# Kernel tuning notes

Measured on AMD Instinct MI355X. Metric: run time of the kernel, lower is better.

The kernel has to match this reference:

```python
import jax, jax.numpy as jnp
import numpy as np

B, T, S, E, H, V, OOV = 16, 32, 400, 128, 512, 32000, 50


def setup_inputs() -> dict:
    key = jax.random.key(0)
    ks = jax.random.split(key, 24)
    sc = 0.05
    inp = {
        'input_embeddings': jax.random.normal(ks[0], (B, T, E), jnp.float32),
        'h0': jax.random.normal(ks[1], (B, H), jnp.float32) * sc,
        'c0': jax.random.normal(ks[2], (B, H), jnp.float32) * sc,
        'encoder_outputs': jax.random.normal(ks[3], (B, S, H), jnp.float32),
        'encoder_masks': jnp.ones((B, S), jnp.float32),
        'extra_zeros': jnp.zeros((B, OOV), jnp.float32),
        'extended_source_idx': jax.random.randint(ks[4], (B, S), 0, V + OOV),
        # LSTM cell params (torch gate order i,f,g,o)
        'W_ih': jax.random.normal(ks[5], (4 * H, E), jnp.float32) * sc,
        'W_hh': jax.random.normal(ks[6], (4 * H, H), jnp.float32) * sc,
        'b_ih': jax.random.normal(ks[7], (4 * H,), jnp.float32) * sc,
        'b_hh': jax.random.normal(ks[8], (4 * H,), jnp.float32) * sc,
        # vocab projection
        'W_vocab': jax.random.normal(ks[9], (V, H), jnp.float32) * sc,
        'b_vocab': jax.random.normal(ks[10], (V,), jnp.float32) * sc,
        # attention: coverage_linear (H,1), energy_linear (H, 2H), v (H)
        'W_cov': jax.random.normal(ks[11], (H, 1), jnp.float32) * sc,
        'W_energy': jax.random.normal(ks[12], (H, 2 * H), jnp.float32) * sc,
        'b_energy': jax.random.normal(ks[13], (H,), jnp.float32) * sc,
        'v_attn': jax.random.uniform(ks[14], (H,), jnp.float32),
        # x_context: (E, E+H)
        'W_xctx': jax.random.normal(ks[15], (E, E + H), jnp.float32) * sc,
        'b_xctx': jax.random.normal(ks[16], (E,), jnp.float32) * sc,
        # attention_dense: (H, 2H)
        'W_ad': jax.random.normal(ks[17], (H, 2 * H), jnp.float32) * sc,
        'b_ad': jax.random.normal(ks[18], (H,), jnp.float32) * sc,
        # p_gen: (1, H + H + E)
        'W_pgen': jax.random.normal(ks[19], (1, 2 * H + E), jnp.float32) * sc,
        'b_pgen': jax.random.normal(ks[20], (1,), jnp.float32) * sc,
    }
    return inp


def _forward(input_embeddings, h0, c0, encoder_outputs, encoder_masks, extra_zeros,
             W_ih, W_hh, b_ih, b_hh, W_vocab, b_vocab, W_cov, W_energy, b_energy,
             v_attn, W_xctx, b_xctx, W_ad, b_ad, W_pgen, b_pgen, extended_source_idx):
    Bc, Sc_, Hc = encoder_outputs.shape
    oov = extra_zeros.shape[1]
    # split energy linear into decoder-part and encoder-part (cat order: [dec, enc])
    W_d, W_e = W_energy[:, :Hc], W_energy[:, Hc:]
    # encoder projection computed ONCE (same math as per-step recompute)
    enc_proj = jnp.einsum('bsh,kh->bsk', encoder_outputs, W_e) + b_energy  # [B,S,H]
    w_cov = W_cov[:, 0]  # [H]
    rows = jnp.arange(Bc)[:, None]

    def step(carry, emb_t):
        h, c, ctx, cov = carry  # [B,H],[B,H],[B,H],[B,S]
        x = jnp.concatenate([emb_t, ctx], -1) @ W_xctx.T + b_xctx  # [B,E]
        gates = x @ W_ih.T + b_ih + h @ W_hh.T + b_hh
        i_g, f_g, g_g, o_g = jnp.split(gates, 4, axis=-1)
        c = jax.nn.sigmoid(f_g) * c + jax.nn.sigmoid(i_g) * jnp.tanh(g_g)
        h = jax.nn.sigmoid(o_g) * jnp.tanh(c)
        # additive attention with coverage
        dec_proj = h @ W_d.T  # [B,H]
        cov_feat = cov[:, :, None] * w_cov[None, None, :]  # [B,S,H]
        energy = jnp.tanh(dec_proj[:, None, :] + enc_proj + cov_feat)
        score = jnp.einsum('bsh,h->bs', energy, v_attn)
        probs = jax.nn.softmax(score, axis=-1) * encoder_masks
        probs = probs / (probs.sum(-1, keepdims=True) + 1e-12)
        ctx = jnp.einsum('bs,bsh->bh', probs, encoder_outputs)
        cov = cov + probs
        # vocab distribution
        hh = jnp.concatenate([h, ctx], -1) @ W_ad.T + b_ad
        vocab_dist = jax.nn.softmax(hh @ W_vocab.T + b_vocab, axis=-1)  # [B,V]
        # pointer-generator mix
        p_gen = jax.nn.sigmoid(jnp.concatenate([ctx, h, x], -1) @ W_pgen.T + b_pgen)  # [B,1]
        attn_ = (1.0 - p_gen) * probs  # [B,S]
        ext = jnp.concatenate([vocab_dist * p_gen, extra_zeros], axis=1)  # [B,V+oov]
        final = ext.at[rows, extended_source_idx].add(attn_)
        return (h, c, ctx, cov), (final, probs, cov)

    init = (h0, c0, jnp.zeros_like(h0), jnp.zeros((Bc, Sc_), h0.dtype))
    (_, _, _, _), (finals, attns, covs) = jax.lax.scan(
        step, init, jnp.swapaxes(input_embeddings, 0, 1))
    return jnp.swapaxes(finals, 0, 1)  # [B,T,V+oov]


def reference(input_embeddings, h0, c0, encoder_outputs, encoder_masks, extra_zeros,
              extended_source_idx, W_ih, W_hh, b_ih, b_hh, W_vocab, b_vocab,
              W_cov, W_energy, b_energy, v_attn, W_xctx, b_xctx, W_ad, b_ad,
              W_pgen, b_pgen):
    return _forward(input_embeddings, h0, c0, encoder_outputs, encoder_masks,
                    extra_zeros, W_ih, W_hh, b_ih, b_hh, W_vocab, b_vocab,
                    W_cov, W_energy, b_energy, v_attn, W_xctx, b_xctx,
                    W_ad, b_ad, W_pgen, b_pgen, extended_source_idx)
```

## Files before the change

### kernel.cpp

```cpp
#include <hip/hip_runtime.h>
#include <hip/hip_bf16.h>
#include <cstddef>

namespace {

constexpr int B = 16, T = 32, S = 400, E = 128, H = 512, V = 32000, OOV = 50, VEXT = V + OOV;

typedef __attribute__((ext_vector_type(8))) short short8v;
typedef __attribute__((ext_vector_type(4))) float f32x4;

__device__ __forceinline__ float fsig(float x){ return 1.0f/(1.0f+__expf(-x)); }
__device__ __forceinline__ float ftanh(float x){
  float ax = fabsf(x);
  float t = __expf(-2.0f*ax);
  float r = (1.0f - t)/(1.0f + t);
  return copysignf(r, x);
}
__device__ __forceinline__ unsigned short f2bf(float f){
  unsigned int u = __float_as_uint(f);
  unsigned int r = (u + 0x7FFFu + ((u >> 16) & 1u)) >> 16;
  return (unsigned short)r;
}
__device__ __forceinline__ float bf2f(unsigned short u){
  return __uint_as_float(((unsigned)u) << 16);
}

__global__ __launch_bounds__(256) void k_init(const float* __restrict__ enc,
    const float* __restrict__ h0, const float* __restrict__ c0,
    unsigned short* __restrict__ enc_bf, float* __restrict__ harr,
    float* __restrict__ cbuf, float* __restrict__ cov, float* __restrict__ vsum){
  const int stride = gridDim.x*256;
  for (int i = blockIdx.x*256 + threadIdx.x; i < B*S*H; i += stride){
    enc_bf[i] = f2bf(enc[i]);
    if (i < B*H){ harr[i] = h0[i]; cbuf[i] = c0[i]; }
    if (i < B*S) cov[i] = 0.0f;
    if (i < T*B) vsum[i] = 0.0f;
  }
}

__global__ __launch_bounds__(128) void k_x0(const float* __restrict__ emb,
    const float* __restrict__ W_xctx, const float* __restrict__ b_xctx,
    float* __restrict__ x0){
  const int b = blockIdx.x, tid = threadIdx.x;
  __shared__ float se[E];
  se[tid] = emb[(size_t)(b*T)*E + tid];
  __syncthreads();
  const float* w = W_xctx + (size_t)tid*(E+H);
  float acc = b_xctx[tid];
  #pragma unroll 8
  for (int k=0;k<E;k+=4){
    float4 wv = *reinterpret_cast<const float4*>(w+k);
    acc += se[k]*wv.x + se[k+1]*wv.y + se[k+2]*wv.z + se[k+3]*wv.w;
  }
  x0[b*E + tid] = acc;
}

__global__ __launch_bounds__(256) void k_trw2(const float* __restrict__ W_energy,
    float* __restrict__ Wt, float* __restrict__ WdT){
  __shared__ float tile[32][33];
  const int z = blockIdx.z;
  float* out = z ? WdT : Wt;
  const int off = z ? 0 : H;
  const int j0 = blockIdx.x*32, k0 = blockIdx.y*32;
  const int tx = threadIdx.x & 31, ty = threadIdx.x >> 5;
  #pragma unroll
  for (int r=0;r<4;++r)
    tile[ty+8*r][tx] = W_energy[(size_t)(k0+ty+8*r)*(2*H) + off + j0 + tx];
  __syncthreads();
  #pragma unroll
  for (int r=0;r<4;++r)
    out[(size_t)(j0+ty+8*r)*H + k0 + tx] = tile[tx][ty+8*r];
}

__global__ __launch_bounds__(512) void k_encproj(const float* __restrict__ enc,
                          const float* __restrict__ Wt,
                          const float* __restrict__ b_energy,
                          unsigned short* __restrict__ enc_proj){
  const int r0 = blockIdx.x*16, k = threadIdx.x;
  const float* eb = enc + (size_t)r0*H;
  float acc[16];
  #pragma unroll
  for (int r=0;r<16;++r) acc[r]=0.0f;
  for (int j=0;j<H;j+=4){
    const float w0 = Wt[(size_t) j   *H + k];
    const float w1 = Wt[(size_t)(j+1)*H + k];
    const float w2 = Wt[(size_t)(j+2)*H + k];
    const float w3 = Wt[(size_t)(j+3)*H + k];
    #pragma unroll
    for (int r=0;r<16;++r){
      acc[r] += eb[(size_t)r*H + j]*w0 + eb[(size_t)r*H + j+1]*w1
              + eb[(size_t)r*H + j+2]*w2 + eb[(size_t)r*H + j+3]*w3;
    }
  }
  const float be = b_energy[k];
  #pragma unroll
  for (int r=0;r<16;++r) enc_proj[(size_t)(r0+r)*H + k] = f2bf(acc[r] + be);
}

__global__ __launch_bounds__(256) void k_gates2(
    const float* __restrict__ x, const float* __restrict__ hold,
    const float* __restrict__ W_ih, const float* __restrict__ W_hh,
    float* __restrict__ gpart){
  const int blk = blockIdx.x, tid = threadIdx.x;
  const int gbh = blk >> 2, kh = blk & 3;
  const int gb = gbh >> 1, bh = gbh & 1, b0 = bh*8;
  __shared__ float xh[8][640];
  __shared__ float sg[4][64][9];
  for (int b=0;b<8;++b)
    for (int k=tid;k<640;k+=256)
      xh[b][k] = (k<E) ? x[(b0+b)*E + k] : hold[(b0+b)*H + (k-E)];
  __syncthreads();
  const int w = tid >> 6, l = tid & 63, g = l >> 4, jj = l & 15;
  const int row = g*H + gb*16 + jj;
  float acc[8];
  #pragma unroll
  for (int b=0;b<8;++b) acc[b]=0.0f;
  const int ks = kh*160 + w*40, ke = ks + 40;
  const int k1 = (ke < 128) ? ke : 128;
  if (ks < 128){
    const float* wr = W_ih + (size_t)row*E;
    for (int k=ks; k<k1; k+=4){
      const float4 wv = *reinterpret_cast<const float4*>(wr + k);
      #pragma unroll
      for (int b=0;b<8;++b){
        const float4 xv = *reinterpret_cast<const float4*>(&xh[b][k]);
        acc[b] += xv.x*wv.x + xv.y*wv.y + xv.z*wv.z + xv.w*wv.w;
      }
    }
  }
  const int k2 = (ks > 128) ? ks : 128;
  if (k2 < ke){
    const float* wr = W_hh + (size_t)row*H - 128;
    for (int k=k2; k<ke; k+=4){
      const float4 wv = *reinterpret_cast<const float4*>(wr + k);
      #pragma unroll
      for (int b=0;b<8;++b){
        const float4 xv = *reinterpret_cast<const float4*>(&xh[b][k]);
        acc[b] += xv.x*wv.x + xv.y*wv.y + xv.z*wv.z + xv.w*wv.w;
      }
    }
  }
  #pragma unroll
  for (int b=0;b<8;++b) sg[w][l][b] = acc[b];
  __syncthreads();
  for (int i=tid; i<512; i+=256){
    const int l2 = i & 63, b = i >> 6;
    const int g2 = l2 >> 4, j2 = l2 & 15;
    const int row2 = g2*H + gb*16 + j2;
    gpart[((size_t)kh*B + (b0+b))*(4*H) + row2] =
        sg[0][l2][b]+sg[1][l2][b]+sg[2][l2][b]+sg[3][l2][b];
  }
}

__global__ __launch_bounds__(256) void k_dec2(const float* __restrict__ gpart,
    const float* __restrict__ cold, const float* __restrict__ b_ih,
    const float* __restrict__ b_hh, const float* __restrict__ WdT,
    float* __restrict__ cnew, float* __restrict__ hnew, float* __restrict__ dec){
  const int blk = blockIdx.x, tid = threadIdx.x;
  const int jc = blk >> 3, bp = blk & 7, b0 = bp*2;
  __shared__ float sh[2][H];
  __shared__ float r[4][64][2];
  for (int i=tid; i<2*H; i+=256){
    const int bl = i >> 9, j = i & 511;
    const int b = b0 + bl;
    float gs[4];
    #pragma unroll
    for (int g=0; g<4; ++g){
      const int row = g*H + j;
      float v = b_ih[row] + b_hh[row];
      #pragma unroll
      for (int kh=0; kh<4; ++kh) v += gpart[((size_t)kh*B + b)*(4*H) + row];
      gs[g] = v;
    }
    const float ig = fsig(gs[0]);
    const float fg = fsig(gs[1]);
    const float gg = ftanh(gs[2]);
    const float og = fsig(gs[3]);
    const float cn = fg*cold[b*H + j] + ig*gg;
    const float hn = og*ftanh(cn);
    cnew[b*H + j] = cn;
    hnew[b*H + j] = hn;
    sh[bl][j] = hn;
  }
  __syncthreads();
  const int w = tid >> 6, lane = tid & 63;
  const int j = jc*64 + lane;
  float a0=0.0f, a1=0.0f;
  for (int k=w*128; k<w*128+128; ++k){
    const float wv = WdT[(size_t)k*H + j];
    a0 += sh[0][k]*wv;
    a1 += sh[1][k]*wv;
  }
  r[w][lane][0]=a0; r[w][lane][1]=a1;
  __syncthreads();
  if (tid < 128){
    const int jl = tid & 63, bb = tid >> 6;
    dec[(b0+bb)*H + jc*64 + jl] = r[0][jl][bb]+r[1][jl][bb]+r[2][jl][bb]+r[3][jl][bb];
  }
}

__global__ __launch_bounds__(256) void k_score(const float* __restrict__ dec_proj,
    const unsigned short* __restrict__ encp, const float* __restrict__ W_cov,
    const float* __restrict__ v_attn, const float* __restrict__ cov,
    float* __restrict__ score, float* __restrict__ xnext){
  const int b = blockIdx.y;
  if (blockIdx.x==0 && threadIdx.x < E) xnext[b*E + threadIdx.x] = 0.0f;
  const int wave = threadIdx.x >> 6, lane = threadIdx.x & 63;
  const int s = blockIdx.x*4 + wave;
  const float cv = cov[b*S + s];
  const int k0 = lane*8;
  const short8v ev = *reinterpret_cast<const short8v*>(encp + (size_t)(b*S + s)*H + k0);
  const float* dp = dec_proj + b*H;
  float acc = 0.0f;
  #pragma unroll
  for (int u=0;u<8;++u){
    const int k = k0+u;
    acc += ftanh(dp[k] + bf2f((unsigned short)ev[u]) + cv*W_cov[k]) * v_attn[k];
  }
  #pragma unroll
  for (int off=32; off>0; off>>=1) acc += __shfl_down(acc, off);
  if (lane==0) score[b*S + s] = acc;
}

__global__ __launch_bounds__(256) void k_ctx(const float* __restrict__ score,
    const float* __restrict__ masks, const unsigned short* __restrict__ enc_bf,
    const float* __restrict__ emb, int tnext,
    const float* __restrict__ W_xctx, const float* __restrict__ b_xctx,
    float* __restrict__ cov, float* __restrict__ probs_t,
    float* __restrict__ ctx_t, float* __restrict__ xnext){
  const int b = blockIdx.x, hc = blockIdx.y, tid = threadIdx.x;
  __shared__ float red[256], sp[512], sctx[64], se[E];
  if (tid < E) se[tid] = emb[(size_t)(b*T + tnext)*E + tid];
  const float sc0 = (tid < S)      ? score[b*S + tid]       : -1e30f;
  const float sc1 = (tid+256 < S)  ? score[b*S + tid + 256] : -1e30f;
  red[tid] = fmaxf(sc0, sc1);
  __syncthreads();
  for (int off=128; off>0; off>>=1){ if (tid<off) red[tid]=fmaxf(red[tid],red[tid+off]); __syncthreads(); }
  const float mx = red[0];
  __syncthreads();
  const float e0 = (tid < S)     ? __expf(sc0 - mx) : 0.0f;
  const float e1 = (tid+256 < S) ? __expf(sc1 - mx) : 0.0f;
  red[tid] = e0 + e1;
  __syncthreads();
  for (int off=128; off>0; off>>=1){ if (tid<off) red[tid]+=red[tid+off]; __syncthreads(); }
  const float den = red[0];
  __syncthreads();
  const float p0 = (tid < S)     ? (e0/den)*masks[b*S+tid]     : 0.0f;
  const float p1 = (tid+256 < S) ? (e1/den)*masks[b*S+tid+256] : 0.0f;
  red[tid] = p0 + p1;
  __syncthreads();
  for (int off=128; off>0; off>>=1){ if (tid<off) red[tid]+=red[tid+off]; __syncthreads(); }
  const float inv = 1.0f/(red[0] + 1e-12f);
  __syncthreads();
  const float pr0 = p0*inv, pr1 = p1*inv;
  sp[tid] = pr0; sp[tid+256] = pr1;
  if (hc==0){
    if (tid < S){ probs_t[b*S+tid] = pr0; cov[b*S+tid] += pr0; }
    if (tid+256 < S){ probs_t[b*S+tid+256] = pr1; cov[b*S+tid+256] += pr1; }
  }
  __syncthreads();
  {
    const int c = tid & 63, sg_ = tid >> 6;
    const unsigned short* eb = enc_bf + (size_t)b*S*H + hc*64 + c;
    float a = 0.0f;
    for (int s=sg_; s<S; s+=4) a += sp[s]*bf2f(eb[(size_t)s*H]);
    red[tid] = a;
    __syncthreads();
    if (tid < 64){
      const float cval = red[tid]+red[tid+64]+red[tid+128]+red[tid+192];
      sctx[tid] = cval;
      ctx_t[b*H + hc*64 + tid] = cval;
    }
  }
  __syncthreads();
  if (tid < E){
    const float* wr = W_xctx + (size_t)tid*(E+H);
    float acc = 0.0f;
    #pragma unroll
    for (int k=0;k<64;k+=4){
      const float4 wc = *reinterpret_cast<const float4*>(wr + E + hc*64 + k);
      acc += sctx[k]*wc.x + sctx[k+1]*wc.y + sctx[k+2]*wc.z + sctx[k+3]*wc.w;
    }
    #pragma unroll
    for (int k=0;k<16;k+=4){
      const float4 we = *reinterpret_cast<const float4*>(wr + hc*16 + k);
      const float* eb2 = se + hc*16 + k;
      acc += eb2[0]*we.x + eb2[1]*we.y + eb2[2]*we.z + eb2[3]*we.w;
    }
    if (hc==0) acc += b_xctx[tid];
    atomicAdd(&xnext[b*E + tid], acc);
  }
}

__global__ __launch_bounds__(512) void k_hhgemm(const float* __restrict__ harr,
    const float* __restrict__ ctx_all, const float* __restrict__ W_ad,
    const float* __restrict__ b_ad, float* __restrict__ hh_all){
  __shared__ unsigned short ldsA[256][72];
  __shared__ unsigned short ldsB[128][72];
  const int tid = threadIdx.x, lane = tid & 63, w = tid >> 6;
  const int wm = w >> 1, wn = w & 1;
  const int m0 = (int)blockIdx.y * 256;
  const int n0 = (int)blockIdx.x * 128;
  const int nl = lane & 15, kg = lane >> 4;
  f32x4 acc[4][4];
  #pragma unroll
  for (int mf=0;mf<4;++mf)
    #pragma unroll
    for (int nf=0;nf<4;++nf) acc[mf][nf] = (f32x4){0.f,0.f,0.f,0.f};
  for (int kc=0; kc<16; ++kc){
    __syncthreads();
    for (int j = tid; j < 4096; j += 512){
      const int row = j >> 4, c4 = j & 15;
      const int kk_ = kc*64 + c4*4;
      const float* src = (kk_ < H)
        ? (harr + (size_t)(m0+row+B)*H + kk_)
        : (ctx_all + (size_t)(m0+row)*H + (kk_ - H));
      const float4 v = *reinterpret_cast<const float4*>(src);
      ushort4 u; u.x=f2bf(v.x); u.y=f2bf(v.y); u.z=f2bf(v.z); u.w=f2bf(v.w);
      *reinterpret_cast<ushort4*>(&ldsA[row][c4*4]) = u;
    }
    for (int j = tid; j < 2048; j += 512){
      const int row = j >> 4, c4 = j & 15;
      const float4 v = *reinterpret_cast<const float4*>(
          W_ad + (size_t)(n0+row)*(2*H) + kc*64 + c4*4);
      ushort4 u; u.x=f2bf(v.x); u.y=f2bf(v.y); u.z=f2bf(v.z); u.w=f2bf(v.w);
      *reinterpret_cast<ushort4*>(&ldsB[row][c4*4]) = u;
    }
    __syncthreads();
    #pragma unroll
    for (int kk=0; kk<2; ++kk){
      short8v a[4], bf[4];
      #pragma unroll
      for (int mf=0;mf<4;++mf)
        a[mf] = *reinterpret_cast<const short8v*>(&ldsA[wm*64 + mf*16 + nl][kk*32 + kg*8]);
      #pragma unroll
      for (int nf=0;nf<4;++nf)
        bf[nf] = *reinterpret_cast<const short8v*>(&ldsB[wn*64 + nf*16 + nl][kk*32 + kg*8]);
      #pragma unroll
      for (int mf=0;mf<4;++mf)
        #pragma unroll
        for (int nf=0;nf<4;++nf)
          acc[mf][nf] = __builtin_amdgcn_mfma_f32_16x16x32_bf16(a[mf], bf[nf], acc[mf][nf], 0, 0, 0);
    }
  }
  #pragma unroll
  for (int mf=0;mf<4;++mf){
    #pragma unroll
    for (int r=0;r<4;++r){
      const int m = m0 + wm*64 + mf*16 + kg*4 + r;
      #pragma unroll
      for (int nf=0;nf<4;++nf){
        const int n = n0 + wn*64 + nf*16 + nl;
        hh_all[(size_t)m*H + n] = acc[mf][nf][r] + b_ad[n];
      }
    }
  }
}

__global__ __launch_bounds__(256) void k_pgen(const float* __restrict__ ctx_all,
    const float* __restrict__ harr, const float* __restrict__ x_all,
    const float* __restrict__ W_pgen, const float* __restrict__ b_pgen,
    float* __restrict__ praw){
  const int wglobal = blockIdx.x*4 + (threadIdx.x >> 6);
  const int lane = threadIdx.x & 63;
  for (int m = wglobal; m < T*B; m += 32){
    float part = 0.0f;
    for (int k = lane; k < 2*H+E; k += 64){
      float v;
      if (k < H)        v = ctx_all[(size_t)m*H + k];
      else if (k < 2*H) v = harr[(size_t)(m+B)*H + (k-H)];
      else              v = x_all[(size_t)m*E + (k-2*H)];
      part += v * W_pgen[k];
    }
    #pragma unroll
    for (int off=32; off>0; off>>=1) part += __shfl_down(part, off);
    if (lane==0) praw[m] = part + b_pgen[0];
  }
}

__global__ __launch_bounds__(512) void k_vocab3(
    const float* __restrict__ hh_all,
    const float* __restrict__ W_vocab, const float* __restrict__ b_vocab,
    float* __restrict__ out, float* __restrict__ vsum){
  __shared__ unsigned short ldsA[256][72];
  __shared__ unsigned short ldsB[128][72];
  __shared__ float svs[256];
  const int tid = threadIdx.x, lane = tid & 63, w = tid >> 6;
  const int wm = w >> 1, wn = w & 1;
  const int m0 = (int)blockIdx.y * 256;
  const int n0 = (int)blockIdx.x * 128;
  const int nl = lane & 15, kg = lane >> 4;
  if (tid < 256) svs[tid] = 0.0f;
  f32x4 acc[4][4];
  #pragma unroll
  for (int mf=0;mf<4;++mf)
    #pragma unroll
    for (int nf=0;nf<4;++nf) acc[mf][nf] = (f32x4){0.f,0.f,0.f,0.f};
  for (int kc=0; kc<8; ++kc){
    __syncthreads();
    for (int j = tid; j < 4096; j += 512){
      const int row = j >> 4, c4 = j & 15;
      const float4 v = *reinterpret_cast<const float4*>(
          hh_all + (size_t)(m0+row)*H + kc*64 + c4*4);
      ushort4 u; u.x=f2bf(v.x); u.y=f2bf(v.y); u.z=f2bf(v.z); u.w=f2bf(v.w);
      *reinterpret_cast<ushort4*>(&ldsA[row][c4*4]) = u;
    }
    for (int j = tid; j < 2048; j += 512){
      const int row = j >> 4, c4 = j & 15;
      const float4 v = *reinterpret_cast<const float4*>(
          W_vocab + (size_t)(n0+row)*H + kc*64 + c4*4);
      ushort4 u; u.x=f2bf(v.x); u.y=f2bf(v.y); u.z=f2bf(v.z); u.w=f2bf(v.w);
      *reinterpret_cast<ushort4*>(&ldsB[row][c4*4]) = u;
    }
    __syncthreads();
    #pragma unroll
    for (int kk=0; kk<2; ++kk){
      short8v a[4], bf[4];
      #pragma unroll
      for (int mf=0;mf<4;++mf)
        a[mf] = *reinterpret_cast<const short8v*>(&ldsA[wm*64 + mf*16 + nl][kk*32 + kg*8]);
      #pragma unroll
      for (int nf=0;nf<4;++nf)
        bf[nf] = *reinterpret_cast<const short8v*>(&ldsB[wn*64 + nf*16 + nl][kk*32 + kg*8]);
      #pragma unroll
      for (int mf=0;mf<4;++mf)
        #pragma unroll
        for (int nf=0;nf<4;++nf)
          acc[mf][nf] = __builtin_amdgcn_mfma_f32_16x16x32_bf16(a[mf], bf[nf], acc[mf][nf], 0, 0, 0);
    }
  }
  float bv[4];
  #pragma unroll
  for (int nf=0;nf<4;++nf) bv[nf] = b_vocab[n0 + wn*64 + nf*16 + nl];
  #pragma unroll
  for (int mf=0;mf<4;++mf){
    #pragma unroll
    for (int r=0;r<4;++r){
      const int m = m0 + wm*64 + mf*16 + kg*4 + r;
      const int tq = m >> 4, bq = m & 15;
      float* orow = out + ((size_t)bq*T + tq)*VEXT;
      float s = 0.0f;
      #pragma unroll
      for (int nf=0;nf<4;++nf){
        const int n = n0 + wn*64 + nf*16 + nl;
        const float e = __expf(acc[mf][nf][r] + bv[nf]);
        orow[n] = e;
        s += e;
      }
      s += __shfl_xor(s, 1);
      s += __shfl_xor(s, 2);
      s += __shfl_xor(s, 4);
      s += __shfl_xor(s, 8);
      if (nl == 0) atomicAdd(&svs[m - m0], s);
    }
  }
  __syncthreads();
  for (int i = tid; i < 256; i += 512) atomicAdd(&vsum[m0 + i], svs[i]);
}

__global__ __launch_bounds__(256) void k_finalize(const float* __restrict__ praw,
    const float* __restrict__ vsum, const float* __restrict__ exz,
    float* __restrict__ out){
  const int rm = blockIdx.x, vc = blockIdx.y, tid = threadIdx.x;
  const int t = rm >> 4, b = rm & 15;
  float* orow = out + ((size_t)b*T + t)*VEXT;
  if (vc < 8){
    const float scl = fsig(praw[rm]) / vsum[rm];
    const int base = vc*4000;
    for (int i = tid; i < 4000; i += 256) orow[base + i] *= scl;
  } else if (tid < OOV){
    orow[V + tid] = exz[b*OOV + tid];
  }
}

__global__ __launch_bounds__(256) void k_scatter_all(const float* __restrict__ probs_all,
    const float* __restrict__ praw, const int* __restrict__ eidx,
    float* __restrict__ out){
  const int stride = gridDim.x*256;
  for (int i = blockIdx.x*256 + threadIdx.x; i < T*B*S; i += stride){
    const int t = i / (B*S);
    const int rem = i - t*B*S;
    const int b = rem / S, s = rem - b*S;
    const float fac = 1.0f - fsig(praw[t*B + b]);
    float* orow = out + ((size_t)b*T + t)*VEXT;
    atomicAdd(&orow[eidx[b*S + s]], fac*probs_all[(size_t)(t*B + b)*S + s]);
  }
}

}

extern "C" void kernel_launch(void* const* d_in, const int* in_sizes, int n_in,
                              void* d_out, int out_size, void* d_ws, size_t ws_size,
                              hipStream_t stream){
  const float* emb    = (const float*)d_in[0];
  const float* h0     = (const float*)d_in[1];
  const float* c0     = (const float*)d_in[2];
  const float* enc    = (const float*)d_in[3];
  const float* masks  = (const float*)d_in[4];
  const float* exz    = (const float*)d_in[5];
  const int*   eidx   = (const int*)d_in[6];
  const float* W_ih   = (const float*)d_in[7];
  const float* W_hh   = (const float*)d_in[8];
  const float* b_ih   = (const float*)d_in[9];
  const float* b_hh   = (const float*)d_in[10];
  const float* W_vocab= (const float*)d_in[11];
  const float* b_vocab= (const float*)d_in[12];
  const float* W_cov  = (const float*)d_in[13];
  const float* W_energy=(const float*)d_in[14];
  const float* b_energy=(const float*)d_in[15];
  const float* v_attn = (const float*)d_in[16];
  const float* W_xctx = (const float*)d_in[17];
  const float* b_xctx = (const float*)d_in[18];
  const float* W_ad   = (const float*)d_in[19];
  const float* b_ad   = (const float*)d_in[20];
  const float* W_pgen = (const float*)d_in[21];
  const float* b_pgen = (const float*)d_in[22];

  float* ws = (float*)d_ws;
  float* cbuf     = ws;
  float* x_all    = ws + 16384;
  float* dec      = ws + 83968;
  float* score    = ws + 92160;
  float* cov      = ws + 98560;
  float* praw     = ws + 104960;
  float* vsum     = ws + 105472;
  float* probs_all= ws + 105984;
  float* harr     = ws + 310784;
  float* ctx_all  = ws + 581120;
  float* hh_all   = ws + 843264;
  float* WdT      = ws + 1105408;
  float* Wt       = ws + 1367552;
  float* gpart    = ws + 1629696;
  unsigned short* enc_bf = (unsigned short*)(ws + 1760768);
  unsigned short* encp   = (unsigned short*)(ws + 3399168);
  float* outp     = (float*)d_out;

  k_init<<<300,256,0,stream>>>(enc,h0,c0,enc_bf,harr,cbuf,cov,vsum);
  k_x0<<<16,128,0,stream>>>(emb,W_xctx,b_xctx,x_all);
  k_trw2<<<dim3(16,16,2),256,0,stream>>>(W_energy,Wt,WdT);
  k_encproj<<<400,512,0,stream>>>(enc,Wt,b_energy,encp);

  for (int t=0;t<T;++t){
    const int p = t&1;
    const float* cold = cbuf + p*8192;
    float* cnew = cbuf + (p^1)*8192;
    const int tnext = (t+1 < T) ? (t+1) : (T-1);
    k_gates2<<<256,256,0,stream>>>(x_all + (size_t)t*B*E, harr + (size_t)t*B*H,
                                   W_ih, W_hh, gpart);
    k_dec2<<<64,256,0,stream>>>(gpart, cold, b_ih, b_hh, WdT,
                                cnew, harr + (size_t)(t+1)*B*H, dec);
    k_score<<<dim3(100,16),256,0,stream>>>(dec, encp, W_cov, v_attn, cov, score,
                                           x_all + (size_t)(t+1)*B*E);
    k_ctx<<<dim3(16,8),256,0,stream>>>(score, masks, enc_bf, emb, tnext,
        W_xctx, b_xctx, cov, probs_all + (size_t)t*B*S,
        ctx_all + (size_t)t*B*H, x_all + (size_t)(t+1)*B*E);
  }

  k_hhgemm<<<dim3(4,2),512,0,stream>>>(harr, ctx_all, W_ad, b_ad, hh_all);
  k_pgen<<<8,256,0,stream>>>(ctx_all, harr, x_all, W_pgen, b_pgen, praw);
  k_vocab3<<<dim3(250,2),512,0,stream>>>(hh_all, W_vocab, b_vocab, outp, vsum);
  k_finalize<<<dim3(512,9),256,0,stream>>>(praw, vsum, exz, outp);
  k_scatter_all<<<200,256,0,stream>>>(probs_all, praw, eidx, outp);
}
```

Baseline: 2.159 ms.

## Fuse recurrent decoder loop into one persistent cooperative kernel with grid syncs

Replaces the 128 per-timestep kernel launches (gates, decoder cell, score, context) with a single cooperative persistent kernel. It uses grid-wide syncs between the gate GEMV phase and a per-batch phase, where one block per batch row computes the LSTM cell, decoder projection, attention, softmax, context and next input. This removes launch overhead and inter-kernel gaps. The cost is that the attention and context work now runs on only 16 blocks instead of hundreds, and each step pays for grid barriers. It also widens k_pgen to one wave per output row.

```diff
diff --git a/kernel.cpp b/kernel.cpp
--- a/kernel.cpp
+++ b/kernel.cpp
@@ -1,6 +1,9 @@
 #include <hip/hip_runtime.h>
 #include <hip/hip_bf16.h>
+#include <hip/hip_cooperative_groups.h>
 #include <cstddef>
+
+namespace cg = cooperative_groups;
 
 namespace {
 
@@ -96,6 +99,7 @@
   #pragma unroll
   for (int r=0;r<16;++r) enc_proj[(size_t)(r0+r)*H + k] = f2bf(acc[r] + be);
 }
+
 
 __global__ __launch_bounds__(256) void k_gates2(
     const float* __restrict__ x, const float* __restrict__ hold,
@@ -292,6 +296,203 @@
   }
 }
 
+
+struct LP {
+  const float *emb, *masks;
+  const float *W_ih, *W_hh, *b_ih, *b_hh;
+  const float *W_cov, *v_attn, *W_xctx, *b_xctx;
+  const float *WdT;
+  const unsigned short *encp, *enc_bf;
+  float *harr, *cbuf, *x_all, *gpart, *cov, *probs_all, *ctx_all;
+};
+
+__global__ __launch_bounds__(256, 1) void fused_loop(LP P){
+  cg::grid_group gg = cg::this_grid();
+  const int blk = blockIdx.x, tid = threadIdx.x;
+  __shared__ union {
+    struct { float xh[8][640]; float sg[4][64][9]; } A;
+    struct { float sh[H]; float sdec[H]; float ss[512]; float sp[512];
+             float sctx[H]; float se[E]; float red[256]; } C;
+  } sm;
+
+  for (int t=0; t<T; ++t){
+    const int p = t&1;
+    const float* cold = P.cbuf + p*8192;
+    float* cnew = P.cbuf + (p^1)*8192;
+    const float* xcur = P.x_all + (size_t)t*B*E;
+    const float* hold = P.harr + (size_t)t*B*H;
+    float* hnew = P.harr + (size_t)(t+1)*B*H;
+    const int tnext = (t+1 < T) ? (t+1) : (T-1);
+
+    {
+      const int gbh = blk >> 2, kh = blk & 3;
+      const int gb = gbh >> 1, bh = gbh & 1, b0 = bh*8;
+      for (int b=0;b<8;++b)
+        for (int k=tid;k<640;k+=256)
+          sm.A.xh[b][k] = (k<E) ? xcur[(b0+b)*E + k] : hold[(b0+b)*H + (k-E)];
+      __syncthreads();
+      const int w = tid >> 6, l = tid & 63, g = l >> 4, jj = l & 15;
+      const int row = g*H + gb*16 + jj;
+      float acc[8];
+      #pragma unroll
+      for (int b=0;b<8;++b) acc[b]=0.0f;
+      const int ks = kh*160 + w*40, ke = ks + 40;
+      const int k1 = (ke < 128) ? ke : 128;
+      if (ks < 128){
+        const float* wr = P.W_ih + (size_t)row*E;
+        for (int k=ks; k<k1; k+=4){
+          const float4 wv = *reinterpret_cast<const float4*>(wr + k);
+          #pragma unroll
+          for (int b=0;b<8;++b){
+            const float4 xv = *reinterpret_cast<const float4*>(&sm.A.xh[b][k]);
+            acc[b] += xv.x*wv.x + xv.y*wv.y + xv.z*wv.z + xv.w*wv.w;
+          }
+        }
+      }
+      const int k2 = (ks > 128) ? ks : 128;
+      if (k2 < ke){
+        const float* wr = P.W_hh + (size_t)row*H - 128;
+        for (int k=k2; k<ke; k+=4){
+          const float4 wv = *reinterpret_cast<const float4*>(wr + k);
+          #pragma unroll
+          for (int b=0;b<8;++b){
+            const float4 xv = *reinterpret_cast<const float4*>(&sm.A.xh[b][k]);
+            acc[b] += xv.x*wv.x + xv.y*wv.y + xv.z*wv.z + xv.w*wv.w;
+          }
+        }
+      }
+      #pragma unroll
+      for (int b=0;b<8;++b) sm.A.sg[w][l][b] = acc[b];
+      __syncthreads();
+      for (int i=tid; i<512; i+=256){
+        const int l2 = i & 63, b = i >> 6;
+        const int g2 = l2 >> 4, j2 = l2 & 15;
+        const int row2 = g2*H + gb*16 + j2;
+        P.gpart[((size_t)kh*B + (b0+b))*(4*H) + row2] =
+            sm.A.sg[0][l2][b]+sm.A.sg[1][l2][b]+sm.A.sg[2][l2][b]+sm.A.sg[3][l2][b];
+      }
+    }
+    gg.sync();
+
+    if (blk < B){
+      const int b = blk;
+      if (tid < E) sm.C.se[tid] = P.emb[(size_t)(b*T + tnext)*E + tid];
+      for (int i=tid; i<H; i+=256){
+        float gs[4];
+        #pragma unroll
+        for (int g=0; g<4; ++g){
+          const int row = g*H + i;
+          float v = P.b_ih[row] + P.b_hh[row];
+          #pragma unroll
+          for (int kh=0; kh<4; ++kh) v += P.gpart[((size_t)kh*B + b)*(4*H) + row];
+          gs[g] = v;
+        }
+        const float ig = fsig(gs[0]);
+        const float fg = fsig(gs[1]);
+        const float g3 = ftanh(gs[2]);
+        const float og = fsig(gs[3]);
+        const float cn = fg*cold[b*H + i] + ig*g3;
+        const float hn = og*ftanh(cn);
+        cnew[b*H + i] = cn;
+        hnew[b*H + i] = hn;
+        sm.C.sh[i] = hn;
+      }
+      __syncthreads();
+      {
+        float a0 = 0.0f, a1 = 0.0f;
+        const int j0 = tid, j1 = tid + 256;
+        for (int k=0; k<H; ++k){
+          const float hv = sm.C.sh[k];
+          const float* wr = P.WdT + (size_t)k*H;
+          a0 += hv*wr[j0];
+          a1 += hv*wr[j1];
+        }
+        sm.C.sdec[j0] = a0;
+        sm.C.sdec[j1] = a1;
+      }
+      __syncthreads();
+      {
+        const int wid = tid >> 6, lane = tid & 63, k0 = lane*8;
+        for (int s = wid; s < S; s += 4){
+          const float cv = P.cov[b*S + s];
+          const short8v ev = *reinterpret_cast<const short8v*>(
+              P.encp + (size_t)(b*S + s)*H + k0);
+          float a = 0.0f;
+          #pragma unroll
+          for (int u=0;u<8;++u){
+            const int k = k0+u;
+            a += ftanh(sm.C.sdec[k] + bf2f((unsigned short)ev[u]) + cv*P.W_cov[k]) * P.v_attn[k];
+          }
+          #pragma unroll
+          for (int off=32; off>0; off>>=1) a += __shfl_down(a, off);
+          if (lane==0) sm.C.ss[s] = a;
+        }
+      }
+      __syncthreads();
+      float* probs_t = P.probs_all + (size_t)t*B*S;
+      const float sc0 = (tid < S)      ? sm.C.ss[tid]       : -1e30f;
+      const float sc1 = (tid+256 < S)  ? sm.C.ss[tid + 256] : -1e30f;
+      sm.C.red[tid] = fmaxf(sc0, sc1);
+      __syncthreads();
+      for (int off=128; off>0; off>>=1){ if (tid<off) sm.C.red[tid]=fmaxf(sm.C.red[tid],sm.C.red[tid+off]); __syncthreads(); }
+      const float mx = sm.C.red[0];
+      __syncthreads();
+      const float e0 = (tid < S)     ? __expf(sc0 - mx) : 0.0f;
+      const float e1 = (tid+256 < S) ? __expf(sc1 - mx) : 0.0f;
+      sm.C.red[tid] = e0 + e1;
+      __syncthreads();
+      for (int off=128; off>0; off>>=1){ if (tid<off) sm.C.red[tid]+=sm.C.red[tid+off]; __syncthreads(); }
+      const float den = sm.C.red[0];
+      __syncthreads();
+      const float p0 = (tid < S)     ? (e0/den)*P.masks[b*S+tid]     : 0.0f;
+      const float p1 = (tid+256 < S) ? (e1/den)*P.masks[b*S+tid+256] : 0.0f;
+      sm.C.red[tid] = p0 + p1;
+      __syncthreads();
+      for (int off=128; off>0; off>>=1){ if (tid<off) sm.C.red[tid]+=sm.C.red[tid+off]; __syncthreads(); }
+      const float inv = 1.0f/(sm.C.red[0] + 1e-12f);
+      __syncthreads();
+      const float pr0 = p0*inv, pr1 = p1*inv;
+      sm.C.sp[tid] = pr0; sm.C.sp[tid+256] = pr1;
+      if (tid < S){ probs_t[b*S+tid] = pr0; P.cov[b*S+tid] += pr0; }
+      if (tid+256 < S){ probs_t[b*S+tid+256] = pr1; P.cov[b*S+tid+256] += pr1; }
+      __syncthreads();
+      {
+        float a0 = 0.0f, a1 = 0.0f;
+        const unsigned short* eb = P.enc_bf + (size_t)b*S*H;
+        for (int s=0; s<S; ++s){
+          const float f = sm.C.sp[s];
+          const unsigned short* row = eb + (size_t)s*H;
+          a0 += f*bf2f(row[tid]);
+          a1 += f*bf2f(row[tid+256]);
+        }
+        sm.C.sctx[tid] = a0;
+        sm.C.sctx[tid+256] = a1;
+        float* ct = P.ctx_all + (size_t)t*B*H + b*H;
+        ct[tid] = a0;
+        ct[tid+256] = a1;
+      }
+      __syncthreads();
+      if (tid < E){
+        const float* wr = P.W_xctx + (size_t)tid*(E+H);
+        float acc = P.b_xctx[tid];
+        #pragma unroll 8
+        for (int k=0;k<E;k+=4){
+          const float4 we = *reinterpret_cast<const float4*>(wr + k);
+          acc += sm.C.se[k]*we.x + sm.C.se[k+1]*we.y + sm.C.se[k+2]*we.z + sm.C.se[k+3]*we.w;
+        }
+        #pragma unroll 8
+        for (int k=0;k<H;k+=4){
+          const float4 wc = *reinterpret_cast<const float4*>(wr + E + k);
+          acc += sm.C.sctx[k]*wc.x + sm.C.sctx[k+1]*wc.y + sm.C.sctx[k+2]*wc.z + sm.C.sctx[k+3]*wc.w;
+        }
+        P.x_all[(size_t)(t+1)*B*E + b*E + tid] = acc;
+      }
+    }
+    gg.sync();
+  }
+}
+
+
 __global__ __launch_bounds__(512) void k_hhgemm(const float* __restrict__ harr,
     const float* __restrict__ ctx_all, const float* __restrict__ W_ad,
     const float* __restrict__ b_ad, float* __restrict__ hh_all){
@@ -361,21 +562,19 @@
     const float* __restrict__ harr, const float* __restrict__ x_all,
     const float* __restrict__ W_pgen, const float* __restrict__ b_pgen,
     float* __restrict__ praw){
-  const int wglobal = blockIdx.x*4 + (threadIdx.x >> 6);
+  const int m = blockIdx.x*4 + (threadIdx.x >> 6);
   const int lane = threadIdx.x & 63;
-  for (int m = wglobal; m < T*B; m += 32){
-    float part = 0.0f;
-    for (int k = lane; k < 2*H+E; k += 64){
-      float v;
-      if (k < H)        v = ctx_all[(size_t)m*H + k];
-      else if (k < 2*H) v = harr[(size_t)(m+B)*H + (k-H)];
-      else              v = x_all[(size_t)m*E + (k-2*H)];
-      part += v * W_pgen[k];
-    }
-    #pragma unroll
-    for (int off=32; off>0; off>>=1) part += __shfl_down(part, off);
-    if (lane==0) praw[m] = part + b_pgen[0];
-  }
+  float part = 0.0f;
+  for (int k = lane; k < 2*H+E; k += 64){
+    float v;
+    if (k < H)        v = ctx_all[(size_t)m*H + k];
+    else if (k < 2*H) v = harr[(size_t)(m+B)*H + (k-H)];
+    else              v = x_all[(size_t)m*E + (k-2*H)];
+    part += v * W_pgen[k];
+  }
+  #pragma unroll
+  for (int off=32; off>0; off>>=1) part += __shfl_down(part, off);
+  if (lane==0) praw[m] = part + b_pgen[0];
 }
 
 __global__ __launch_bounds__(512) void k_vocab3(
@@ -540,24 +739,43 @@
   k_trw2<<<dim3(16,16,2),256,0,stream>>>(W_energy,Wt,WdT);
   k_encproj<<<400,512,0,stream>>>(enc,Wt,b_energy,encp);
 
-  for (int t=0;t<T;++t){
-    const int p = t&1;
-    const float* cold = cbuf + p*8192;
-    float* cnew = cbuf + (p^1)*8192;
-    const int tnext = (t+1 < T) ? (t+1) : (T-1);
-    k_gates2<<<256,256,0,stream>>>(x_all + (size_t)t*B*E, harr + (size_t)t*B*H,
-                                   W_ih, W_hh, gpart);
-    k_dec2<<<64,256,0,stream>>>(gpart, cold, b_ih, b_hh, WdT,
-                                cnew, harr + (size_t)(t+1)*B*H, dec);
-    k_score<<<dim3(100,16),256,0,stream>>>(dec, encp, W_cov, v_attn, cov, score,
-                                           x_all + (size_t)(t+1)*B*E);
-    k_ctx<<<dim3(16,8),256,0,stream>>>(score, masks, enc_bf, emb, tnext,
-        W_xctx, b_xctx, cov, probs_all + (size_t)t*B*S,
-        ctx_all + (size_t)t*B*H, x_all + (size_t)(t+1)*B*E);
+  int occ = 0;
+  hipError_t occErr = hipOccupancyMaxActiveBlocksPerMultiprocessor(
+      &occ, (const void*)fused_loop, 256, 0);
+  bool coop = (occErr == hipSuccess && occ >= 1);
+  if (coop){
+    LP P;
+    P.emb=emb; P.masks=masks;
+    P.W_ih=W_ih; P.W_hh=W_hh; P.b_ih=b_ih; P.b_hh=b_hh;
+    P.W_cov=W_cov; P.v_attn=v_attn; P.W_xctx=W_xctx; P.b_xctx=b_xctx;
+    P.WdT=WdT; P.encp=encp; P.enc_bf=enc_bf;
+    P.harr=harr; P.cbuf=cbuf; P.x_all=x_all; P.gpart=gpart;
+    P.cov=cov; P.probs_all=probs_all; P.ctx_all=ctx_all;
+    void* args[] = { (void*)&P };
+    hipError_t lerr = hipLaunchCooperativeKernel((const void*)fused_loop,
+        dim3(256), dim3(256), args, 0, stream);
+    if (lerr != hipSuccess) coop = false;
+  }
+  if (!coop){
+    for (int t=0;t<T;++t){
+      const int p = t&1;
+      const float* cold = cbuf + p*8192;
+      float* cnew = cbuf + (p^1)*8192;
+      const int tnext = (t+1 < T) ? (t+1) : (T-1);
+      k_gates2<<<256,256,0,stream>>>(x_all + (size_t)t*B*E, harr + (size_t)t*B*H,
+                                     W_ih, W_hh, gpart);
+      k_dec2<<<64,256,0,stream>>>(gpart, cold, b_ih, b_hh, WdT,
+                                  cnew, harr + (size_t)(t+1)*B*H, dec);
+      k_score<<<dim3(100,16),256,0,stream>>>(dec, encp, W_cov, v_attn, cov, score,
+                                             x_all + (size_t)(t+1)*B*E);
+      k_ctx<<<dim3(16,8),256,0,stream>>>(score, masks, enc_bf, emb, tnext,
+          W_xctx, b_xctx, cov, probs_all + (size_t)t*B*S,
+          ctx_all + (size_t)t*B*H, x_all + (size_t)(t+1)*B*E);
+    }
   }
 
   k_hhgemm<<<dim3(4,2),512,0,stream>>>(harr, ctx_all, W_ad, b_ad, hh_all);
-  k_pgen<<<8,256,0,stream>>>(ctx_all, harr, x_all, W_pgen, b_pgen, praw);
+  k_pgen<<<128,256,0,stream>>>(ctx_all, harr, x_all, W_pgen, b_pgen, praw);
   k_vocab3<<<dim3(250,2),512,0,stream>>>(hh_all, W_vocab, b_vocab, outp, vsum);
   k_finalize<<<dim3(512,9),256,0,stream>>>(praw, vsum, exz, outp);
   k_scatter_all<<<200,256,0,stream>>>(probs_all, praw, eidx, outp);
```

After: 6.432 ms. +197.9%, slower.

## Fuse LSTM cell, attention scores and context into one per-batch step kernel

Applied to the files above, without the earlier changes.

Replaces three per-timestep kernels (k_dec2, k_score and k_ctx) with a single k_step kernel that uses one 512-thread block per batch row. Inside that block it computes the LSTM cell update, the decoder projection, the attention scores, the softmax, the context vector and the next input. This removes two launches per step, the global round trips for dec and score, and the atomicAdd/zeroing of xnext. The cost is much less parallelism: only 16 blocks, with long serial per-thread loops over 512 k values and 400 s values. It also spreads k_pgen across 128 blocks with one row per wave instead of a strided loop.

```diff
diff --git a/kernel.cpp b/kernel.cpp
--- a/kernel.cpp
+++ b/kernel.cpp
@@ -152,17 +152,22 @@
   }
 }
 
-__global__ __launch_bounds__(256) void k_dec2(const float* __restrict__ gpart,
-    const float* __restrict__ cold, const float* __restrict__ b_ih,
-    const float* __restrict__ b_hh, const float* __restrict__ WdT,
-    float* __restrict__ cnew, float* __restrict__ hnew, float* __restrict__ dec){
-  const int blk = blockIdx.x, tid = threadIdx.x;
-  const int jc = blk >> 3, bp = blk & 7, b0 = bp*2;
-  __shared__ float sh[2][H];
-  __shared__ float r[4][64][2];
-  for (int i=tid; i<2*H; i+=256){
-    const int bl = i >> 9, j = i & 511;
-    const int b = b0 + bl;
+__global__ __launch_bounds__(512) void k_step(
+    const float* __restrict__ gpart, const float* __restrict__ cold,
+    const float* __restrict__ b_ih, const float* __restrict__ b_hh,
+    const float* __restrict__ WdT, const unsigned short* __restrict__ encp,
+    const float* __restrict__ W_cov, const float* __restrict__ v_attn,
+    const unsigned short* __restrict__ enc_bf, const float* __restrict__ masks,
+    const float* __restrict__ emb, int tnext,
+    const float* __restrict__ W_xctx, const float* __restrict__ b_xctx,
+    float* __restrict__ cov, float* __restrict__ probs_t,
+    float* __restrict__ ctx_t, float* __restrict__ cnew,
+    float* __restrict__ hnew, float* __restrict__ xnext){
+  const int b = blockIdx.x, tid = threadIdx.x;
+  __shared__ float sh[H], sdec[H], sctx[H], swc[H], sva[H];
+  __shared__ float ss[512], sp[512], red[512], se[E];
+  {
+    const int j = tid;
     float gs[4];
     #pragma unroll
     for (int g=0; g<4; ++g){
@@ -180,115 +185,84 @@
     const float hn = og*ftanh(cn);
     cnew[b*H + j] = cn;
     hnew[b*H + j] = hn;
-    sh[bl][j] = hn;
-  }
-  __syncthreads();
-  const int w = tid >> 6, lane = tid & 63;
-  const int j = jc*64 + lane;
-  float a0=0.0f, a1=0.0f;
-  for (int k=w*128; k<w*128+128; ++k){
-    const float wv = WdT[(size_t)k*H + j];
-    a0 += sh[0][k]*wv;
-    a1 += sh[1][k]*wv;
-  }
-  r[w][lane][0]=a0; r[w][lane][1]=a1;
-  __syncthreads();
-  if (tid < 128){
-    const int jl = tid & 63, bb = tid >> 6;
-    dec[(b0+bb)*H + jc*64 + jl] = r[0][jl][bb]+r[1][jl][bb]+r[2][jl][bb]+r[3][jl][bb];
-  }
-}
-
-__global__ __launch_bounds__(256) void k_score(const float* __restrict__ dec_proj,
-    const unsigned short* __restrict__ encp, const float* __restrict__ W_cov,
-    const float* __restrict__ v_attn, const float* __restrict__ cov,
-    float* __restrict__ score, float* __restrict__ xnext){
-  const int b = blockIdx.y;
-  if (blockIdx.x==0 && threadIdx.x < E) xnext[b*E + threadIdx.x] = 0.0f;
-  const int wave = threadIdx.x >> 6, lane = threadIdx.x & 63;
-  const int s = blockIdx.x*4 + wave;
-  const float cv = cov[b*S + s];
-  const int k0 = lane*8;
-  const short8v ev = *reinterpret_cast<const short8v*>(encp + (size_t)(b*S + s)*H + k0);
-  const float* dp = dec_proj + b*H;
-  float acc = 0.0f;
-  #pragma unroll
-  for (int u=0;u<8;++u){
-    const int k = k0+u;
-    acc += ftanh(dp[k] + bf2f((unsigned short)ev[u]) + cv*W_cov[k]) * v_attn[k];
-  }
-  #pragma unroll
-  for (int off=32; off>0; off>>=1) acc += __shfl_down(acc, off);
-  if (lane==0) score[b*S + s] = acc;
-}
-
-__global__ __launch_bounds__(256) void k_ctx(const float* __restrict__ score,
-    const float* __restrict__ masks, const unsigned short* __restrict__ enc_bf,
-    const float* __restrict__ emb, int tnext,
-    const float* __restrict__ W_xctx, const float* __restrict__ b_xctx,
-    float* __restrict__ cov, float* __restrict__ probs_t,
-    float* __restrict__ ctx_t, float* __restrict__ xnext){
-  const int b = blockIdx.x, hc = blockIdx.y, tid = threadIdx.x;
-  __shared__ float red[256], sp[512], sctx[64], se[E];
+    sh[j] = hn;
+    swc[j] = W_cov[j];
+    sva[j] = v_attn[j];
+  }
   if (tid < E) se[tid] = emb[(size_t)(b*T + tnext)*E + tid];
-  const float sc0 = (tid < S)      ? score[b*S + tid]       : -1e30f;
-  const float sc1 = (tid+256 < S)  ? score[b*S + tid + 256] : -1e30f;
-  red[tid] = fmaxf(sc0, sc1);
-  __syncthreads();
-  for (int off=128; off>0; off>>=1){ if (tid<off) red[tid]=fmaxf(red[tid],red[tid+off]); __syncthreads(); }
+  __syncthreads();
+  {
+    float a = 0.0f;
+    #pragma unroll 4
+    for (int k=0; k<H; ++k) a += sh[k] * WdT[(size_t)k*H + tid];
+    sdec[tid] = a;
+  }
+  __syncthreads();
+  {
+    const int wid = tid >> 6, lane = tid & 63, k0 = lane*8;
+    for (int s = wid; s < S; s += 8){
+      const float cv = cov[b*S + s];
+      const short8v ev = *reinterpret_cast<const short8v*>(
+          encp + (size_t)(b*S + s)*H + k0);
+      float a = 0.0f;
+      #pragma unroll
+      for (int u=0;u<8;++u){
+        const int k = k0+u;
+        a += ftanh(sdec[k] + bf2f((unsigned short)ev[u]) + cv*swc[k]) * sva[k];
+      }
+      #pragma unroll
+      for (int off=32; off>0; off>>=1) a += __shfl_down(a, off);
+      if (lane==0) ss[s] = a;
+    }
+  }
+  __syncthreads();
+  const float sc = (tid < S) ? ss[tid] : -1e30f;
+  red[tid] = sc;
+  __syncthreads();
+  for (int off=256; off>0; off>>=1){ if (tid<off) red[tid]=fmaxf(red[tid],red[tid+off]); __syncthreads(); }
   const float mx = red[0];
   __syncthreads();
-  const float e0 = (tid < S)     ? __expf(sc0 - mx) : 0.0f;
-  const float e1 = (tid+256 < S) ? __expf(sc1 - mx) : 0.0f;
-  red[tid] = e0 + e1;
-  __syncthreads();
-  for (int off=128; off>0; off>>=1){ if (tid<off) red[tid]+=red[tid+off]; __syncthreads(); }
+  const float ev_ = (tid < S) ? __expf(sc - mx) : 0.0f;
+  red[tid] = ev_;
+  __syncthreads();
+  for (int off=256; off>0; off>>=1){ if (tid<off) red[tid]+=red[tid+off]; __syncthreads(); }
   const float den = red[0];
   __syncthreads();
-  const float p0 = (tid < S)     ? (e0/den)*masks[b*S+tid]     : 0.0f;
-  const float p1 = (tid+256 < S) ? (e1/den)*masks[b*S+tid+256] : 0.0f;
-  red[tid] = p0 + p1;
-  __syncthreads();
-  for (int off=128; off>0; off>>=1){ if (tid<off) red[tid]+=red[tid+off]; __syncthreads(); }
+  const float p = (tid < S) ? (ev_/den)*masks[b*S+tid] : 0.0f;
+  red[tid] = p;
+  __syncthreads();
+  for (int off=256; off>0; off>>=1){ if (tid<off) red[tid]+=red[tid+off]; __syncthreads(); }
   const float inv = 1.0f/(red[0] + 1e-12f);
   __syncthreads();
-  const float pr0 = p0*inv, pr1 = p1*inv;
-  sp[tid] = pr0; sp[tid+256] = pr1;
-  if (hc==0){
-    if (tid < S){ probs_t[b*S+tid] = pr0; cov[b*S+tid] += pr0; }
-    if (tid+256 < S){ probs_t[b*S+tid+256] = pr1; cov[b*S+tid+256] += pr1; }
+  const float pr = p*inv;
+  sp[tid] = pr;
+  if (tid < S){
+    probs_t[b*S + tid] = pr;
+    cov[b*S + tid] += pr;
   }
   __syncthreads();
   {
-    const int c = tid & 63, sg_ = tid >> 6;
-    const unsigned short* eb = enc_bf + (size_t)b*S*H + hc*64 + c;
     float a = 0.0f;
-    for (int s=sg_; s<S; s+=4) a += sp[s]*bf2f(eb[(size_t)s*H]);
-    red[tid] = a;
-    __syncthreads();
-    if (tid < 64){
-      const float cval = red[tid]+red[tid+64]+red[tid+128]+red[tid+192];
-      sctx[tid] = cval;
-      ctx_t[b*H + hc*64 + tid] = cval;
-    }
+    const unsigned short* eb = enc_bf + (size_t)b*S*H + tid;
+    for (int s=0; s<S; ++s) a += sp[s]*bf2f(eb[(size_t)s*H]);
+    sctx[tid] = a;
+    ctx_t[b*H + tid] = a;
   }
   __syncthreads();
   if (tid < E){
     const float* wr = W_xctx + (size_t)tid*(E+H);
-    float acc = 0.0f;
-    #pragma unroll
-    for (int k=0;k<64;k+=4){
-      const float4 wc = *reinterpret_cast<const float4*>(wr + E + hc*64 + k);
+    float acc = b_xctx[tid];
+    #pragma unroll 8
+    for (int k=0;k<E;k+=4){
+      const float4 we = *reinterpret_cast<const float4*>(wr + k);
+      acc += se[k]*we.x + se[k+1]*we.y + se[k+2]*we.z + se[k+3]*we.w;
+    }
+    #pragma unroll 8
+    for (int k=0;k<H;k+=4){
+      const float4 wc = *reinterpret_cast<const float4*>(wr + E + k);
       acc += sctx[k]*wc.x + sctx[k+1]*wc.y + sctx[k+2]*wc.z + sctx[k+3]*wc.w;
     }
-    #pragma unroll
-    for (int k=0;k<16;k+=4){
-      const float4 we = *reinterpret_cast<const float4*>(wr + hc*16 + k);
-      const float* eb2 = se + hc*16 + k;
-      acc += eb2[0]*we.x + eb2[1]*we.y + eb2[2]*we.z + eb2[3]*we.w;
-    }
-    if (hc==0) acc += b_xctx[tid];
-    atomicAdd(&xnext[b*E + tid], acc);
+    xnext[b*E + tid] = acc;
   }
 }
 
@@ -361,21 +335,19 @@
     const float* __restrict__ harr, const float* __restrict__ x_all,
     const float* __restrict__ W_pgen, const float* __restrict__ b_pgen,
     float* __restrict__ praw){
-  const int wglobal = blockIdx.x*4 + (threadIdx.x >> 6);
+  const int m = blockIdx.x*4 + (threadIdx.x >> 6);
   const int lane = threadIdx.x & 63;
-  for (int m = wglobal; m < T*B; m += 32){
-    float part = 0.0f;
-    for (int k = lane; k < 2*H+E; k += 64){
-      float v;
-      if (k < H)        v = ctx_all[(size_t)m*H + k];
-      else if (k < 2*H) v = harr[(size_t)(m+B)*H + (k-H)];
-      else              v = x_all[(size_t)m*E + (k-2*H)];
-      part += v * W_pgen[k];
-    }
-    #pragma unroll
-    for (int off=32; off>0; off>>=1) part += __shfl_down(part, off);
-    if (lane==0) praw[m] = part + b_pgen[0];
-  }
+  float part = 0.0f;
+  for (int k = lane; k < 2*H+E; k += 64){
+    float v;
+    if (k < H)        v = ctx_all[(size_t)m*H + k];
+    else if (k < 2*H) v = harr[(size_t)(m+B)*H + (k-H)];
+    else              v = x_all[(size_t)m*E + (k-2*H)];
+    part += v * W_pgen[k];
+  }
+  #pragma unroll
+  for (int off=32; off>0; off>>=1) part += __shfl_down(part, off);
+  if (lane==0) praw[m] = part + b_pgen[0];
 }
 
 __global__ __launch_bounds__(512) void k_vocab3(
@@ -519,20 +491,18 @@
   float* ws = (float*)d_ws;
   float* cbuf     = ws;
   float* x_all    = ws + 16384;
-  float* dec      = ws + 83968;
-  float* score    = ws + 92160;
-  float* cov      = ws + 98560;
-  float* praw     = ws + 104960;
-  float* vsum     = ws + 105472;
-  float* probs_all= ws + 105984;
-  float* harr     = ws + 310784;
-  float* ctx_all  = ws + 581120;
-  float* hh_all   = ws + 843264;
-  float* WdT      = ws + 1105408;
-  float* Wt       = ws + 1367552;
-  float* gpart    = ws + 1629696;
-  unsigned short* enc_bf = (unsigned short*)(ws + 1760768);
-  unsigned short* encp   = (unsigned short*)(ws + 3399168);
+  float* cov      = ws + 83968;
+  float* praw     = ws + 90368;
+  float* vsum     = ws + 90880;
+  float* probs_all= ws + 91392;
+  float* harr     = ws + 296192;
+  float* ctx_all  = ws + 566528;
+  float* hh_all   = ws + 828672;
+  float* WdT      = ws + 1090816;
+  float* Wt       = ws + 1352960;
+  float* gpart    = ws + 1615104;
+  unsigned short* enc_bf = (unsigned short*)(ws + 1746176);
+  unsigned short* encp   = (unsigned short*)(ws + 3384576);
   float* outp     = (float*)d_out;
 
   k_init<<<300,256,0,stream>>>(enc,h0,c0,enc_bf,harr,cbuf,cov,vsum);
@@ -547,17 +517,14 @@
     const int tnext = (t+1 < T) ? (t+1) : (T-1);
     k_gates2<<<256,256,0,stream>>>(x_all + (size_t)t*B*E, harr + (size_t)t*B*H,
                                    W_ih, W_hh, gpart);
-    k_dec2<<<64,256,0,stream>>>(gpart, cold, b_ih, b_hh, WdT,
-                                cnew, harr + (size_t)(t+1)*B*H, dec);
-    k_score<<<dim3(100,16),256,0,stream>>>(dec, encp, W_cov, v_attn, cov, score,
-                                           x_all + (size_t)(t+1)*B*E);
-    k_ctx<<<dim3(16,8),256,0,stream>>>(score, masks, enc_bf, emb, tnext,
-        W_xctx, b_xctx, cov, probs_all + (size_t)t*B*S,
-        ctx_all + (size_t)t*B*H, x_all + (size_t)(t+1)*B*E);
+    k_step<<<16,512,0,stream>>>(gpart, cold, b_ih, b_hh, WdT, encp, W_cov, v_attn,
+        enc_bf, masks, emb, tnext, W_xctx, b_xctx,
+        cov, probs_all + (size_t)t*B*S, ctx_all + (size_t)t*B*H,
+        cnew, harr + (size_t)(t+1)*B*H, x_all + (size_t)(t+1)*B*E);
   }
 
   k_hhgemm<<<dim3(4,2),512,0,stream>>>(harr, ctx_all, W_ad, b_ad, hh_all);
-  k_pgen<<<8,256,0,stream>>>(ctx_all, harr, x_all, W_pgen, b_pgen, praw);
+  k_pgen<<<128,256,0,stream>>>(ctx_all, harr, x_all, W_pgen, b_pgen, praw);
   k_vocab3<<<dim3(250,2),512,0,stream>>>(hh_all, W_vocab, b_vocab, outp, vsum);
   k_finalize<<<dim3(512,9),256,0,stream>>>(praw, vsum, exz, outp);
   k_scatter_all<<<200,256,0,stream>>>(probs_all, praw, eidx, outp);
```

Result: slower. 4.177 ms (+93.5%).
